# Performance work log

Hardware: AMD Instinct MI355X
Metric: run time of the kernel (lower is better)

The kernel has to match this reference:

```python
import jax, jax.numpy as jnp
import numpy as np

N_NODES = 100000
N_EDGES = 1600000
D = 64
N_LAYERS = 5
N_GRAPHS = 256


def setup_inputs() -> dict:
    key = jax.random.key(0)
    ks = jax.random.split(key, 12)
    x = jax.random.normal(ks[0], (N_NODES, D), dtype=jnp.float32)
    edge_index = jax.random.randint(ks[1], (2, N_EDGES), 0, N_NODES, dtype=jnp.int64)
    batch = jnp.sort(jax.random.randint(ks[2], (N_NODES,), 0, N_GRAPHS, dtype=jnp.int64))
    s = 1.0 / np.sqrt(D)
    # stacked GINConv MLP params: Linear(D,D) -> ReLU -> Linear(D,D), per layer
    Ws1 = jax.random.uniform(ks[3], (N_LAYERS, D, D), jnp.float32, -s, s)
    bs1 = jax.random.uniform(ks[4], (N_LAYERS, D), jnp.float32, -s, s)
    Ws2 = jax.random.uniform(ks[5], (N_LAYERS, D, D), jnp.float32, -s, s)
    bs2 = jax.random.uniform(ks[6], (N_LAYERS, D), jnp.float32, -s, s)
    # final readout MLP: Linear(D,D) -> ReLU -> Linear(D,D)
    mW1 = jax.random.uniform(ks[7], (D, D), jnp.float32, -s, s)
    mb1 = jax.random.uniform(ks[8], (D,), jnp.float32, -s, s)
    mW2 = jax.random.uniform(ks[9], (D, D), jnp.float32, -s, s)
    mb2 = jax.random.uniform(ks[10], (D,), jnp.float32, -s, s)
    return {"x": x, "edge_index": edge_index, "batch": batch,
            "Ws1": Ws1, "bs1": bs1, "Ws2": Ws2, "bs2": bs2,
            "mW1": mW1, "mb1": mb1, "mW2": mW2, "mb2": mb2}


def reference(x, edge_index, batch, Ws1, bs1, Ws2, bs2, mW1, mb1, mW2, mb2):
    src, dst = edge_index[0], edge_index[1]
    h = x
    for l in range(N_LAYERS):
        # GINConv (eps=0): MLP(h + sum_{j in N(i)} h_j)
        agg = jax.ops.segment_sum(h[src], dst, num_segments=N_NODES)
        z = h + agg
        z = jax.nn.relu(z @ Ws1[l] + bs1[l])
        h = z @ Ws2[l] + bs2[l]
    # global mean pool over graphs
    sums = jax.ops.segment_sum(h, batch, num_segments=N_GRAPHS)
    cnts = jax.ops.segment_sum(jnp.ones((h.shape[0],), h.dtype), batch, num_segments=N_GRAPHS)
    pooled = sums / jnp.maximum(cnts, 1.0)[:, None]
    # readout MLP
    out = jax.nn.relu(pooled @ mW1 + mb1) @ mW2 + mb2
    return out
```

## Files before the change

kernel.cpp:

```cpp
#include <hip/hip_runtime.h>
#include <hip/hip_bf16.h>

#define N_NODES 100000
#define N_EDGES 1600000
#define DIM 64
#define N_LAYERS 5
#define N_GRAPHS 256

#define NB2 196
#define SUBCAP2 9216
#define CAP2 12800
#define DUMMY N_NODES
#define TILE 3200
#define NTILE 500
#define MTILES (N_NODES / 16)

typedef __attribute__((ext_vector_type(8))) short short8;
typedef __attribute__((ext_vector_type(4))) float float4v;

__global__ void zero_kernel(int* p, int n) {
    int i = blockIdx.x * blockDim.x + threadIdx.x;
    if (i < n) p[i] = 0;
}

__device__ __forceinline__ unsigned short f2bf(float f) {
    unsigned int u = __float_as_uint(f);
    unsigned int r = (u + 0x7fffu + ((u >> 16) & 1u)) >> 16;
    return (unsigned short)r;
}
__device__ __forceinline__ float bf2f(unsigned short b) {
    return __uint_as_float(((unsigned int)b) << 16);
}

__global__ void zero_dummy_kernel(unsigned short* a, unsigned short* b) {
    int t = threadIdx.x;
    a[(size_t)DUMMY * DIM + t] = 0;
    b[(size_t)DUMMY * DIM + t] = 0;
}

__global__ void cvt_kernel(const float4* __restrict__ x, ushort4* __restrict__ hb, int n4) {
    int i = blockIdx.x * blockDim.x + threadIdx.x;
    if (i < n4) {
        float4 v = x[i];
        ushort4 o;
        o.x = f2bf(v.x); o.y = f2bf(v.y); o.z = f2bf(v.z); o.w = f2bf(v.w);
        hb[i] = o;
    }
}

__global__ void prepack_kernel(const float* __restrict__ Ws1, const float* __restrict__ Ws2,
                               unsigned short* __restrict__ wpk) {
    int t = blockIdx.x * blockDim.x + threadIdx.x;
    if (t >= N_LAYERS * 32 * 64) return;
    int lane = t & 63;
    int frag = (t >> 6) & 31;
    int l = t >> 11;
    int kf = frag & 1;
    int nt = (frag >> 1) & 3;
    int split = (frag >> 3) & 1;
    int mat = (frag >> 4) & 1;
    const float* W = (mat ? Ws2 : Ws1) + (size_t)l * DIM * DIM;
    unsigned short outv[8];
#pragma unroll
    for (int j = 0; j < 8; ++j) {
        int k = kf * 32 + ((lane >> 4) << 3) + j;
        int n = nt * 16 + (lane & 15);
        float v = W[k * DIM + n];
        unsigned short hi = f2bf(v);
        outv[j] = split ? f2bf(v - bf2f(hi)) : hi;
    }
    ushort4* dst = (ushort4*)(wpk + ((size_t)(l * 32 + frag) * 64 + lane) * 8);
    dst[0] = make_ushort4(outv[0], outv[1], outv[2], outv[3]);
    dst[1] = make_ushort4(outv[4], outv[5], outv[6], outv[7]);
}

__global__ __launch_bounds__(256) void bin_kernel(
    const int* __restrict__ src, const int* __restrict__ dst,
    int* __restrict__ bcursor, int* __restrict__ pairbuf) {
    __shared__ int hcnt[NB2];
    __shared__ int gbase[NB2];
    __shared__ int lcur[NB2];
    const int tid = threadIdx.x;
    const int base = blockIdx.x * TILE;

    for (int l = tid; l < NB2; l += 256) { hcnt[l] = 0; lcur[l] = 0; }
    __syncthreads();
    for (int j = tid; j < TILE; j += 256) {
        int d = dst[base + j];
        atomicAdd(&hcnt[d >> 9], 1);
    }
    __syncthreads();
    for (int l = tid; l < NB2; l += 256)
        gbase[l] = atomicAdd(&bcursor[l], hcnt[l]);
    __syncthreads();
    for (int j = tid; j < TILE; j += 256) {
        int s = src[base + j];
        int d = dst[base + j];
        int b = d >> 9;
        int r = atomicAdd(&lcur[b], 1);
        int pos = gbase[b] + r;
        if (pos < SUBCAP2) pairbuf[b * SUBCAP2 + pos] = (s << 9) | (d & 511);
    }
}

__global__ __launch_bounds__(256) void csr_kernel(
    const int* __restrict__ bcursor, const int* __restrict__ pairbuf,
    int* __restrict__ esrc, int2* __restrict__ meta) {
    __shared__ int lcnt[512];
    __shared__ int loff[512];
    __shared__ int lcur[512];
    __shared__ int s2[256];
    const int b = blockIdx.x;
    const int tid = threadIdx.x;
    int ec = bcursor[b];
    if (ec > SUBCAP2) ec = SUBCAP2;
    const int* pp = pairbuf + b * SUBCAP2;

    for (int l = tid; l < 512; l += 256) lcnt[l] = 0;
    __syncthreads();
    for (int j = tid; j < ec; j += 256) atomicAdd(&lcnt[pp[j] & 511], 1);
    __syncthreads();

    int c0 = (lcnt[2 * tid] + 7) & ~7;
    int c1 = (lcnt[2 * tid + 1] + 7) & ~7;
    s2[tid] = c0 + c1;
    __syncthreads();
    for (int off = 1; off < 256; off <<= 1) {
        int v = (tid >= off) ? s2[tid - off] : 0;
        __syncthreads();
        s2[tid] += v;
        __syncthreads();
    }
    int exc = s2[tid] - (c0 + c1);
    loff[2 * tid] = exc;
    loff[2 * tid + 1] = exc + c0;
    __syncthreads();

    int* eb = esrc + (size_t)b * CAP2;
    for (int l = tid; l < 512; l += 256) {
        int st = loff[l];
        int cn = lcnt[l];
        int cp = (cn + 7) & ~7;
        lcur[l] = st;
        int node = b * 512 + l;
        if (node < N_NODES) meta[node] = make_int2(b * CAP2 + st, cp);
        for (int j = cn; j < cp; ++j) eb[st + j] = DUMMY;
    }
    __syncthreads();

    for (int j = tid; j < ec; j += 256) {
        int p = pp[j];
        int pos = atomicAdd(&lcur[p & 511], 1);
        eb[pos] = p >> 9;
    }
}

__device__ __forceinline__ void acc8(float* acc, uint4 v) {
    acc[0] += __uint_as_float(v.x << 16);
    acc[1] += __uint_as_float(v.x & 0xffff0000u);
    acc[2] += __uint_as_float(v.y << 16);
    acc[3] += __uint_as_float(v.y & 0xffff0000u);
    acc[4] += __uint_as_float(v.z << 16);
    acc[5] += __uint_as_float(v.z & 0xffff0000u);
    acc[6] += __uint_as_float(v.w << 16);
    acc[7] += __uint_as_float(v.w & 0xffff0000u);
}

typedef const __attribute__((address_space(1))) void* as1cv;
typedef __attribute__((address_space(3))) void* as3v;
__device__ __forceinline__ void gload16(const void* g, void* l) {
    __builtin_amdgcn_global_load_lds((as1cv)g, (as3v)l, 16, 0, 0);
}

__global__ __launch_bounds__(256) void agg_kernel(
    const unsigned short* __restrict__ hin, unsigned short* __restrict__ z,
    const int2* __restrict__ meta, const int* __restrict__ esrc, int n_nodes) {
    __shared__ char scratch[4][4096];
    const int lane = threadIdx.x & 63;
    const int wv = threadIdx.x >> 6;
    const int grp = lane >> 3;
    const int sub = lane & 7;
    const int wave_id = (blockIdx.x * blockDim.x + threadIdx.x) >> 6;
    const int n_waves = (gridDim.x * blockDim.x) >> 6;
    char* ring = scratch[wv];
    const char* hb = (const char*)hin;

    for (int ii = wave_id; 2 * ii < n_nodes; ii += n_waves) {
        const int iA = 2 * ii;
        const int iB = iA + 1;
        const int2 mA = meta[iA];
        const int2 mB = meta[iB];
        const float selfA = bf2f(hin[(size_t)iA * DIM + lane]);
        const float selfB = bf2f(hin[(size_t)iB * DIM + lane]);
        const int nA = mA.y, nB = mB.y;
        const int* eA = esrc + mA.x + grp;
        const int* eB = esrc + mB.x + grp;
        const int nb = ((nA > nB) ? nA : nB) >> 3;

        float accA[8] = {0.f, 0.f, 0.f, 0.f, 0.f, 0.f, 0.f, 0.f};
        float accB[8] = {0.f, 0.f, 0.f, 0.f, 0.f, 0.f, 0.f, 0.f};

        if (nb > 0) {
            int o;
            o = (0 < nA) ? 0 : 0;
            int ia0 = eA[o]; ia0 = (0 < nA) ? ia0 : DUMMY;
            int ib0 = eB[o]; ib0 = (0 < nB) ? ib0 : DUMMY;
            o = (8 < nA) ? 8 : 0;
            int ia1 = eA[o]; ia1 = (8 < nA) ? ia1 : DUMMY;
            o = (8 < nB) ? 8 : 0;
            int ib1 = eB[o]; ib1 = (8 < nB) ? ib1 : DUMMY;
            asm volatile("s_waitcnt lgkmcnt(0)" ::: "memory");
            gload16(hb + ((size_t)(unsigned)ia0 << 7) + (sub << 4), ring);
            gload16(hb + ((size_t)(unsigned)ib0 << 7) + (sub << 4), ring + 2048);
            if (nb > 1) {
                gload16(hb + ((size_t)(unsigned)ia1 << 7) + (sub << 4), ring + 1024);
                gload16(hb + ((size_t)(unsigned)ib1 << 7) + (sub << 4), ring + 3072);
            }
            asm volatile("" ::: "memory");
            int t8 = 16;
            int oA = (t8 < nA) ? t8 : 0;
            int oB = (t8 < nB) ? t8 : 0;
            int nxA = eA[oA]; nxA = (t8 < nA) ? nxA : DUMMY;
            int nxB = eB[oB]; nxB = (t8 < nB) ? nxB : DUMMY;

            for (int b = 0; b < nb; ++b) {
                if (b + 1 < nb) asm volatile("s_waitcnt vmcnt(4)" ::: "memory");
                else            asm volatile("s_waitcnt vmcnt(2)" ::: "memory");
                const int s = (b & 1) << 10;
                uint4 va = *(const uint4*)(ring + s + lane * 16);
                uint4 vb = *(const uint4*)(ring + 2048 + s + lane * 16);
                acc8(accA, va);
                acc8(accB, vb);
                if (b + 2 < nb) {
                    asm volatile("s_waitcnt lgkmcnt(0)" ::: "memory");
                    gload16(hb + ((size_t)(unsigned)nxA << 7) + (sub << 4), ring + s);
                    gload16(hb + ((size_t)(unsigned)nxB << 7) + (sub << 4), ring + 2048 + s);
                    asm volatile("" ::: "memory");
                    t8 = 8 * (b + 3);
                    oA = (t8 < nA) ? t8 : 0;
                    oB = (t8 < nB) ? t8 : 0;
                    nxA = eA[oA]; nxA = (t8 < nA) ? nxA : DUMMY;
                    nxB = eB[oB]; nxB = (t8 < nB) ? nxB : DUMMY;
                }
            }
        }

        float* zbA = (float*)ring;
        float* zbB = (float*)(ring + 2048);
        *((float4*)&zbA[grp * 64 + sub * 8 + 0]) = make_float4(accA[0], accA[1], accA[2], accA[3]);
        *((float4*)&zbA[grp * 64 + sub * 8 + 4]) = make_float4(accA[4], accA[5], accA[6], accA[7]);
        *((float4*)&zbB[grp * 64 + sub * 8 + 0]) = make_float4(accB[0], accB[1], accB[2], accB[3]);
        *((float4*)&zbB[grp * 64 + sub * 8 + 4]) = make_float4(accB[4], accB[5], accB[6], accB[7]);
        __builtin_amdgcn_wave_barrier();
        float zA = selfA, zB = selfB;
#pragma unroll
        for (int g = 0; g < 8; ++g) {
            zA += zbA[g * 64 + lane];
            zB += zbB[g * 64 + lane];
        }
        z[(size_t)iA * DIM + lane] = f2bf(zA);
        z[(size_t)iB * DIM + lane] = f2bf(zB);
        __builtin_amdgcn_wave_barrier();
    }
}

__device__ __forceinline__ short8 load_frag(const unsigned short* __restrict__ wl, int frag, int lane) {
    union { uint4 u; short8 s; } c;
    c.u = *(const uint4*)(wl + ((size_t)(frag * 64 + lane)) * 8);
    return c.s;
}

__device__ __forceinline__ void split8(const float* v, short8& hi, short8& lo) {
#pragma unroll
    for (int j = 0; j < 8; ++j) {
        unsigned short h = f2bf(v[j]);
        hi[j] = (short)h;
        lo[j] = (short)f2bf(v[j] - bf2f(h));
    }
}

__global__ __launch_bounds__(256) void mlp_mfma_kernel(
    const unsigned short* __restrict__ z, unsigned short* __restrict__ hout,
    const unsigned short* __restrict__ wl,
    const float* __restrict__ b1, const float* __restrict__ b2) {
    __shared__ float tbuf[4][16][68];
    const int lane = threadIdx.x & 63;
    const int wv = threadIdx.x >> 6;
    const int m = lane & 15;
    const int quad = lane >> 4;
    const int wave_id = (blockIdx.x * blockDim.x + threadIdx.x) >> 6;
    const int n_waves = (gridDim.x * blockDim.x) >> 6;

    float b1v[4], b2v[4];
#pragma unroll
    for (int nt = 0; nt < 4; ++nt) {
        b1v[nt] = b1[nt * 16 + m];
        b2v[nt] = b2[nt * 16 + m];
    }

    for (int tile = wave_id; tile < MTILES; tile += n_waves) {
        const int node0 = tile * 16;

        short8 a1[2];
#pragma unroll
        for (int kf = 0; kf < 2; ++kf) {
            union { uint4 u; short8 s; } c;
            c.u = *(const uint4*)(z + ((size_t)(node0 + m)) * DIM + kf * 32 + quad * 8);
            a1[kf] = c.s;
        }

        float4v acc1[4] = {};
#pragma unroll
        for (int nt = 0; nt < 4; ++nt) {
#pragma unroll
            for (int kf = 0; kf < 2; ++kf) {
                short8 bhi = load_frag(wl, ((0 * 2 + 0) * 4 + nt) * 2 + kf, lane);
                short8 blo = load_frag(wl, ((0 * 2 + 1) * 4 + nt) * 2 + kf, lane);
                acc1[nt] = __builtin_amdgcn_mfma_f32_16x16x32_bf16(a1[kf], bhi, acc1[nt], 0, 0, 0);
                acc1[nt] = __builtin_amdgcn_mfma_f32_16x16x32_bf16(a1[kf], blo, acc1[nt], 0, 0, 0);
            }
        }

#pragma unroll
        for (int nt = 0; nt < 4; ++nt) {
#pragma unroll
            for (int r = 0; r < 4; ++r) {
                float tv = acc1[nt][r] + b1v[nt];
                tbuf[wv][quad * 4 + r][nt * 16 + m] = fmaxf(tv, 0.f);
            }
        }
        __builtin_amdgcn_wave_barrier();

        short8 a2hi[2], a2lo[2];
#pragma unroll
        for (int kf = 0; kf < 2; ++kf) {
            const float4* tp = (const float4*)&tbuf[wv][m][kf * 32 + quad * 8];
            float4 t0 = tp[0];
            float4 t1 = tp[1];
            float v[8] = {t0.x, t0.y, t0.z, t0.w, t1.x, t1.y, t1.z, t1.w};
            split8(v, a2hi[kf], a2lo[kf]);
        }
        __builtin_amdgcn_wave_barrier();

        float4v acc2[4] = {};
#pragma unroll
        for (int nt = 0; nt < 4; ++nt) {
#pragma unroll
            for (int kf = 0; kf < 2; ++kf) {
                short8 bhi = load_frag(wl, ((1 * 2 + 0) * 4 + nt) * 2 + kf, lane);
                short8 blo = load_frag(wl, ((1 * 2 + 1) * 4 + nt) * 2 + kf, lane);
                acc2[nt] = __builtin_amdgcn_mfma_f32_16x16x32_bf16(a2hi[kf], bhi, acc2[nt], 0, 0, 0);
                acc2[nt] = __builtin_amdgcn_mfma_f32_16x16x32_bf16(a2hi[kf], blo, acc2[nt], 0, 0, 0);
                acc2[nt] = __builtin_amdgcn_mfma_f32_16x16x32_bf16(a2lo[kf], bhi, acc2[nt], 0, 0, 0);
            }
        }

#pragma unroll
        for (int nt = 0; nt < 4; ++nt) {
#pragma unroll
            for (int r = 0; r < 4; ++r) {
                float o = acc2[nt][r] + b2v[nt];
                hout[((size_t)(node0 + quad * 4 + r)) * DIM + nt * 16 + m] = f2bf(o);
            }
        }
    }
}

__global__ __launch_bounds__(256) void pool_mlp_kernel(
    const unsigned short* __restrict__ h, const int* __restrict__ batch,
    const float* __restrict__ mW1, const float* __restrict__ mb1,
    const float* __restrict__ mW2, const float* __restrict__ mb2,
    float* __restrict__ out, int n_nodes) {
    __shared__ float part[4][DIM];
    const int g = blockIdx.x;
    const int lane = threadIdx.x & 63;
    const int w = threadIdx.x >> 6;

    int lo = 0, hi = n_nodes;
    while (lo < hi) {
        int mid = (lo + hi) >> 1;
        if (batch[mid] < g) lo = mid + 1; else hi = mid;
    }
    const int s0 = lo;
    hi = n_nodes;
    while (lo < hi) {
        int mid = (lo + hi) >> 1;
        if (batch[mid] < g + 1) lo = mid + 1; else hi = mid;
    }
    const int e0 = lo;

    float acc = 0.f;
    int i = s0 + w;
    for (; i + 12 < e0; i += 16) {
        float v0 = bf2f(h[i * DIM + lane]);
        float v1 = bf2f(h[(i + 4) * DIM + lane]);
        float v2 = bf2f(h[(i + 8) * DIM + lane]);
        float v3 = bf2f(h[(i + 12) * DIM + lane]);
        acc += (v0 + v1) + (v2 + v3);
    }
    for (; i < e0; i += 4) acc += bf2f(h[i * DIM + lane]);
    part[w][lane] = acc;
    __syncthreads();

    if (w == 0) {
        acc = (part[0][lane] + part[1][lane]) + (part[2][lane] + part[3][lane]);
        float cntf = (float)(e0 - s0);
        acc /= fmaxf(cntf, 1.f);

        float t = mb1[lane];
#pragma unroll
        for (int d = 0; d < DIM; ++d) {
            float zd = __shfl(acc, d);
            t = fmaf(zd, mW1[d * DIM + lane], t);
        }
        t = fmaxf(t, 0.f);
        float o = mb2[lane];
#pragma unroll
        for (int d = 0; d < DIM; ++d) {
            float rd = __shfl(t, d);
            o = fmaf(rd, mW2[d * DIM + lane], o);
        }
        out[g * DIM + lane] = o;
    }
}

extern "C" void kernel_launch(void* const* d_in, const int* in_sizes, int n_in,
                              void* d_out, int out_size, void* d_ws, size_t ws_size,
                              hipStream_t stream) {
    const float* x   = (const float*)d_in[0];
    const int*   ei  = (const int*)d_in[1];
    const int*   bat = (const int*)d_in[2];
    const float* Ws1 = (const float*)d_in[3];
    const float* bs1 = (const float*)d_in[4];
    const float* Ws2 = (const float*)d_in[5];
    const float* bs2 = (const float*)d_in[6];
    const float* mW1 = (const float*)d_in[7];
    const float* mb1 = (const float*)d_in[8];
    const float* mW2 = (const float*)d_in[9];
    const float* mb2 = (const float*)d_in[10];
    float* out = (float*)d_out;

    char* ws = (char*)d_ws;
    size_t off = 0;
    auto alloc = [&](size_t bytes) {
        void* p = ws + off;
        off += (bytes + 255) & ~(size_t)255;
        return p;
    };
    int*  esrc    = (int*)alloc((size_t)NB2 * CAP2 * 4);
    int2* meta    = (int2*)alloc((size_t)N_NODES * 8);
    unsigned short* hbfA = (unsigned short*)alloc(((size_t)N_NODES + 1) * DIM * 2);
    unsigned short* hbfB = (unsigned short*)alloc(((size_t)N_NODES + 1) * DIM * 2);
    int*  bcursor = (int*)alloc((size_t)NB2 * 4);
    unsigned short* wpk = (unsigned short*)alloc((size_t)N_LAYERS * 32 * 64 * 8 * 2);
    int*   pairbuf = (int*)alloc((size_t)NB2 * SUBCAP2 * 4);
    unsigned short* zbig = (unsigned short*)alloc((size_t)N_NODES * DIM * 2);

    const int* src = ei;
    const int* dst = ei + N_EDGES;

    zero_kernel<<<1, 256, 0, stream>>>(bcursor, NB2);
    bin_kernel<<<NTILE, 256, 0, stream>>>(src, dst, bcursor, pairbuf);
    csr_kernel<<<NB2, 256, 0, stream>>>(bcursor, pairbuf, esrc, meta);

    prepack_kernel<<<(N_LAYERS * 32 * 64 + 255) / 256, 256, 0, stream>>>(Ws1, Ws2, wpk);
    zero_dummy_kernel<<<1, 64, 0, stream>>>(hbfA, hbfB);
    cvt_kernel<<<(N_NODES * DIM / 4 + 255) / 256, 256, 0, stream>>>(
        (const float4*)x, (ushort4*)hbfA, N_NODES * DIM / 4);

    const unsigned short* hin = hbfA;
    unsigned short* hout = hbfB;
    for (int l = 0; l < N_LAYERS; ++l) {
        agg_kernel<<<2048, 256, 0, stream>>>(hin, zbig, meta, esrc, N_NODES);
        mlp_mfma_kernel<<<1024, 256, 0, stream>>>(zbig, hout,
                                                  wpk + (size_t)l * 32 * 64 * 8,
                                                  bs1 + (size_t)l * DIM,
                                                  bs2 + (size_t)l * DIM);
        hin = hout;
        hout = (hout == hbfA) ? hbfB : hbfA;
    }
    pool_mlp_kernel<<<N_GRAPHS, 256, 0, stream>>>(hin, bat, mW1, mb1, mW2, mb2, out, N_NODES);
}
```

Baseline: 372.0 us.

## Fuse setup kernels, halve CSR bucket size, and double MLP grid

```diff
diff --git a/kernel.cpp b/kernel.cpp
--- a/kernel.cpp
+++ b/kernel.cpp
@@ -7,21 +7,22 @@
 #define N_LAYERS 5
 #define N_GRAPHS 256
 
-#define NB2 196
-#define SUBCAP2 9216
-#define CAP2 12800
+#define NB2 391
+#define BSH 8
+#define BMSK 255
+#define SUBCAP2 4608
+#define CAP2 6400
 #define DUMMY N_NODES
 #define TILE 3200
 #define NTILE 500
 #define MTILES (N_NODES / 16)
 
+#define CVT_BLOCKS 6250
+#define PREPACK_BLOCKS 40
+#define SETUP_BLOCKS (CVT_BLOCKS + PREPACK_BLOCKS + 1)
+
 typedef __attribute__((ext_vector_type(8))) short short8;
 typedef __attribute__((ext_vector_type(4))) float float4v;
-
-__global__ void zero_kernel(int* p, int n) {
-    int i = blockIdx.x * blockDim.x + threadIdx.x;
-    if (i < n) p[i] = 0;
-}
 
 __device__ __forceinline__ unsigned short f2bf(float f) {
     unsigned int u = __float_as_uint(f);
@@ -32,46 +33,48 @@
     return __uint_as_float(((unsigned int)b) << 16);
 }
 
-__global__ void zero_dummy_kernel(unsigned short* a, unsigned short* b) {
-    int t = threadIdx.x;
-    a[(size_t)DUMMY * DIM + t] = 0;
-    b[(size_t)DUMMY * DIM + t] = 0;
-}
-
-__global__ void cvt_kernel(const float4* __restrict__ x, ushort4* __restrict__ hb, int n4) {
-    int i = blockIdx.x * blockDim.x + threadIdx.x;
-    if (i < n4) {
+__global__ __launch_bounds__(256) void setup_kernel(
+    const float4* __restrict__ x, ushort4* __restrict__ hb,
+    const float* __restrict__ Ws1, const float* __restrict__ Ws2,
+    unsigned short* __restrict__ wpk, int* __restrict__ bcursor,
+    unsigned short* __restrict__ hA, unsigned short* __restrict__ hB) {
+    const int b = blockIdx.x;
+    const int tid = threadIdx.x;
+    if (b < CVT_BLOCKS) {
+        int i = b * 256 + tid;
         float4 v = x[i];
         ushort4 o;
         o.x = f2bf(v.x); o.y = f2bf(v.y); o.z = f2bf(v.z); o.w = f2bf(v.w);
         hb[i] = o;
-    }
-}
-
-__global__ void prepack_kernel(const float* __restrict__ Ws1, const float* __restrict__ Ws2,
-                               unsigned short* __restrict__ wpk) {
-    int t = blockIdx.x * blockDim.x + threadIdx.x;
-    if (t >= N_LAYERS * 32 * 64) return;
-    int lane = t & 63;
-    int frag = (t >> 6) & 31;
-    int l = t >> 11;
-    int kf = frag & 1;
-    int nt = (frag >> 1) & 3;
-    int split = (frag >> 3) & 1;
-    int mat = (frag >> 4) & 1;
-    const float* W = (mat ? Ws2 : Ws1) + (size_t)l * DIM * DIM;
-    unsigned short outv[8];
-#pragma unroll
-    for (int j = 0; j < 8; ++j) {
-        int k = kf * 32 + ((lane >> 4) << 3) + j;
-        int n = nt * 16 + (lane & 15);
-        float v = W[k * DIM + n];
-        unsigned short hi = f2bf(v);
-        outv[j] = split ? f2bf(v - bf2f(hi)) : hi;
-    }
-    ushort4* dst = (ushort4*)(wpk + ((size_t)(l * 32 + frag) * 64 + lane) * 8);
-    dst[0] = make_ushort4(outv[0], outv[1], outv[2], outv[3]);
-    dst[1] = make_ushort4(outv[4], outv[5], outv[6], outv[7]);
+    } else if (b < CVT_BLOCKS + PREPACK_BLOCKS) {
+        int t = (b - CVT_BLOCKS) * 256 + tid;
+        int lane = t & 63;
+        int frag = (t >> 6) & 31;
+        int l = t >> 11;
+        int kf = frag & 1;
+        int nt = (frag >> 1) & 3;
+        int split = (frag >> 3) & 1;
+        int mat = (frag >> 4) & 1;
+        const float* W = (mat ? Ws2 : Ws1) + (size_t)l * DIM * DIM;
+        unsigned short outv[8];
+#pragma unroll
+        for (int j = 0; j < 8; ++j) {
+            int k = kf * 32 + ((lane >> 4) << 3) + j;
+            int n = nt * 16 + (lane & 15);
+            float v = W[k * DIM + n];
+            unsigned short hi = f2bf(v);
+            outv[j] = split ? f2bf(v - bf2f(hi)) : hi;
+        }
+        ushort4* dst = (ushort4*)(wpk + ((size_t)(l * 32 + frag) * 64 + lane) * 8);
+        dst[0] = make_ushort4(outv[0], outv[1], outv[2], outv[3]);
+        dst[1] = make_ushort4(outv[4], outv[5], outv[6], outv[7]);
+    } else {
+        for (int l = tid; l < NB2; l += 256) bcursor[l] = 0;
+        if (tid < DIM) {
+            hA[(size_t)DUMMY * DIM + tid] = 0;
+            hB[(size_t)DUMMY * DIM + tid] = 0;
+        }
+    }
 }
 
 __global__ __launch_bounds__(256) void bin_kernel(
@@ -87,7 +90,7 @@
     __syncthreads();
     for (int j = tid; j < TILE; j += 256) {
         int d = dst[base + j];
-        atomicAdd(&hcnt[d >> 9], 1);
+        atomicAdd(&hcnt[d >> BSH], 1);
     }
     __syncthreads();
     for (int l = tid; l < NB2; l += 256)
@@ -96,19 +99,19 @@
     for (int j = tid; j < TILE; j += 256) {
         int s = src[base + j];
         int d = dst[base + j];
-        int b = d >> 9;
+        int b = d >> BSH;
         int r = atomicAdd(&lcur[b], 1);
         int pos = gbase[b] + r;
-        if (pos < SUBCAP2) pairbuf[b * SUBCAP2 + pos] = (s << 9) | (d & 511);
-    }
-}
-
-__global__ __launch_bounds__(256) void csr_kernel(
+        if (pos < SUBCAP2) pairbuf[b * SUBCAP2 + pos] = (s << BSH) | (d & BMSK);
+    }
+}
+
+__global__ __launch_bounds__(512) void csr_kernel(
     const int* __restrict__ bcursor, const int* __restrict__ pairbuf,
     int* __restrict__ esrc, int2* __restrict__ meta) {
-    __shared__ int lcnt[512];
-    __shared__ int loff[512];
-    __shared__ int lcur[512];
+    __shared__ int lcnt[256];
+    __shared__ int loff[256];
+    __shared__ int lcur[256];
     __shared__ int s2[256];
     const int b = blockIdx.x;
     const int tid = threadIdx.x;
@@ -116,42 +119,42 @@
     if (ec > SUBCAP2) ec = SUBCAP2;
     const int* pp = pairbuf + b * SUBCAP2;
 
-    for (int l = tid; l < 512; l += 256) lcnt[l] = 0;
-    __syncthreads();
-    for (int j = tid; j < ec; j += 256) atomicAdd(&lcnt[pp[j] & 511], 1);
-    __syncthreads();
-
-    int c0 = (lcnt[2 * tid] + 7) & ~7;
-    int c1 = (lcnt[2 * tid + 1] + 7) & ~7;
-    s2[tid] = c0 + c1;
+    if (tid < 256) lcnt[tid] = 0;
+    __syncthreads();
+    for (int j = tid; j < ec; j += 512) atomicAdd(&lcnt[pp[j] & BMSK], 1);
+    __syncthreads();
+
+    if (tid < 256) s2[tid] = (lcnt[tid] + 7) & ~7;
     __syncthreads();
     for (int off = 1; off < 256; off <<= 1) {
-        int v = (tid >= off) ? s2[tid - off] : 0;
+        int v = (tid >= off && tid < 256) ? s2[tid - off] : 0;
         __syncthreads();
-        s2[tid] += v;
+        if (tid < 256) s2[tid] += v;
         __syncthreads();
     }
-    int exc = s2[tid] - (c0 + c1);
-    loff[2 * tid] = exc;
-    loff[2 * tid + 1] = exc + c0;
+    if (tid < 256) {
+        int c = (lcnt[tid] + 7) & ~7;
+        int exc = s2[tid] - c;
+        loff[tid] = exc;
+        lcur[tid] = exc;
+    }
     __syncthreads();
 
     int* eb = esrc + (size_t)b * CAP2;
-    for (int l = tid; l < 512; l += 256) {
+    for (int l = tid; l < 256; l += 512) {
         int st = loff[l];
         int cn = lcnt[l];
         int cp = (cn + 7) & ~7;
-        lcur[l] = st;
-        int node = b * 512 + l;
+        int node = b * 256 + l;
         if (node < N_NODES) meta[node] = make_int2(b * CAP2 + st, cp);
         for (int j = cn; j < cp; ++j) eb[st + j] = DUMMY;
     }
     __syncthreads();
 
-    for (int j = tid; j < ec; j += 256) {
+    for (int j = tid; j < ec; j += 512) {
         int p = pp[j];
-        int pos = atomicAdd(&lcur[p & 511], 1);
-        eb[pos] = p >> 9;
+        int pos = atomicAdd(&lcur[p & BMSK], 1);
+        eb[pos] = p >> BSH;
     }
 }
 
@@ -459,20 +462,17 @@
     const int* src = ei;
     const int* dst = ei + N_EDGES;
 
-    zero_kernel<<<1, 256, 0, stream>>>(bcursor, NB2);
+    setup_kernel<<<SETUP_BLOCKS, 256, 0, stream>>>(
+        (const float4*)x, (ushort4*)hbfA, Ws1, Ws2, wpk, bcursor, hbfA, hbfB);
+
     bin_kernel<<<NTILE, 256, 0, stream>>>(src, dst, bcursor, pairbuf);
-    csr_kernel<<<NB2, 256, 0, stream>>>(bcursor, pairbuf, esrc, meta);
-
-    prepack_kernel<<<(N_LAYERS * 32 * 64 + 255) / 256, 256, 0, stream>>>(Ws1, Ws2, wpk);
-    zero_dummy_kernel<<<1, 64, 0, stream>>>(hbfA, hbfB);
-    cvt_kernel<<<(N_NODES * DIM / 4 + 255) / 256, 256, 0, stream>>>(
-        (const float4*)x, (ushort4*)hbfA, N_NODES * DIM / 4);
+    csr_kernel<<<NB2, 512, 0, stream>>>(bcursor, pairbuf, esrc, meta);
 
     const unsigned short* hin = hbfA;
     unsigned short* hout = hbfB;
     for (int l = 0; l < N_LAYERS; ++l) {
         agg_kernel<<<2048, 256, 0, stream>>>(hin, zbig, meta, esrc, N_NODES);
-        mlp_mfma_kernel<<<1024, 256, 0, stream>>>(zbig, hout,
+        mlp_mfma_kernel<<<2048, 256, 0, stream>>>(zbig, hout,
                                                   wpk + (size_t)l * 32 * 64 * 8,
                                                   bs1 + (size_t)l * DIM,
                                                   bs2 + (size_t)l * DIM);
```

New measurement: 371.4 us (median of 2 runs). No clear change (-0.2%).
